# Optimization experiments

Measured on AMD Instinct MI355X. Metric: run time of the kernel, lower is better.

## Reference

```python
import jax, jax.numpy as jnp
import numpy as np

B, H, I, E = 16, 16, 512, 512  # batch, heads, input_dim, embedding_dim (I must == E for matmul(q,k))


def setup_inputs() -> dict:
    key = jax.random.key(0)
    k_x, k_q, k_k, k_v, k_w, k_b = jax.random.split(key, 6)
    return {
        "x": jax.random.normal(k_x, (B, 1, I, E), dtype=jnp.float32),
        "W_q": jax.random.normal(k_q, (1, H, I, E), dtype=jnp.float32),
        "W_k": jax.random.normal(k_k, (1, H, I, E), dtype=jnp.float32),
        "W_v": jax.random.normal(k_v, (1, H, I, E), dtype=jnp.float32),
        "mlp_w": jax.random.normal(k_w, (E, E), dtype=jnp.float32) * (1.0 / np.sqrt(E)),
        "mlp_b": jnp.zeros((E,), dtype=jnp.float32),
    }


def reference(x, W_q, W_k, W_v, mlp_w, mlp_b):
    # Broadcast elementwise "projections": [B,1,I,E] * [1,H,I,E] -> [B,H,I,E]
    q = x * W_q
    k = x * W_k
    v = x * W_v
    scale = jnp.sqrt(jnp.asarray(E, dtype=x.dtype))
    # matmul with NO transpose of keys (as in the original): [B,H,I,E]@[B,H,I,E] needs E==I
    scores = jnp.matmul(q, k) / scale            # [B,H,I,I]
    attn = jax.nn.softmax(scores, axis=2)        # softmax over dim=2 (rows), faithful to source
    emb = jnp.sum(jnp.matmul(attn, v), axis=2)   # [B,H,I,E] summed over I -> [B,H,E]
    return emb @ mlp_w.T + mlp_b                 # nn.Linear: x @ W^T + b -> [B,H,E]
```

## Files before the change

kernel.cpp:

```cpp
#include <hip/hip_runtime.h>

#define B_ 16
#define H_ 16
#define I_ 512
#define E_ 512


#define NSLICE 16
#define KSPLIT 8

__global__ __launch_bounds__(256) void k_emb_part(const float* __restrict__ x,
                                                  const float* __restrict__ Wv,
                                                  float* __restrict__ part) {
    const int etile = blockIdx.x;
    const int slice = blockIdx.y;
    const int t     = (int)threadIdx.x;
    const int lane  = t & 63;
    const int wave  = t >> 6;
    const int e     = etile * 64 + lane;
    const int b0    = (wave & 1) * 8;
    const int h0    = (wave >> 1) * 8;

    __shared__ float xs[8][16][64];
    __shared__ float ws[8][16][64];

    float acc[8][8];
#pragma unroll
    for (int bi = 0; bi < 8; ++bi)
#pragma unroll
        for (int hj = 0; hj < 8; ++hj) acc[bi][hj] = 0.0f;

    const int ibase0 = slice * 32;

    for (int chunk = 0; chunk < 4; ++chunk) {
        const int ib = ibase0 + chunk * 8;
        if (chunk) __syncthreads();
#pragma unroll
        for (int it2 = 0; it2 < 8; ++it2) {
            const int f  = t + it2 * 256;
            const int ii = f >> 8;
            const int bb = (f >> 4) & 15;
            const int eq = f & 15;
            const size_t goff = ((size_t)bb * I_ + (ib + ii)) * E_ + etile * 64 + eq * 4;
            float4 vx = *(const float4*)(x + goff);
            float4 vw = *(const float4*)(Wv + goff);
            *(float4*)&xs[ii][bb][eq * 4] = vx;
            *(float4*)&ws[ii][bb][eq * 4] = vw;
        }
        __syncthreads();

#pragma unroll
        for (int ii = 0; ii < 8; ++ii) {
            float xv[8], wv[8];
#pragma unroll
            for (int bi = 0; bi < 8; ++bi) xv[bi] = xs[ii][b0 + bi][lane];
#pragma unroll
            for (int hj = 0; hj < 8; ++hj) wv[hj] = ws[ii][h0 + hj][lane];
#pragma unroll
            for (int bi = 0; bi < 8; ++bi)
#pragma unroll
                for (int hj = 0; hj < 8; ++hj)
                    acc[bi][hj] = fmaf(xv[bi], wv[hj], acc[bi][hj]);
        }
    }

#pragma unroll
    for (int bi = 0; bi < 8; ++bi)
#pragma unroll
        for (int hj = 0; hj < 8; ++hj) {
            const int row = (b0 + bi) * H_ + h0 + hj;
            part[((size_t)slice * (B_ * H_) + row) * E_ + e] = acc[bi][hj];
        }
}

__global__ __launch_bounds__(256) void k_emb_reduce(const float4* __restrict__ part,
                                                    float4* __restrict__ emb) {
    const int idx = blockIdx.x * 256 + threadIdx.x;
    const int sl  = (B_ * H_ * E_) / 4;
    float4 s = part[idx];
#pragma unroll
    for (int j = 1; j < NSLICE; ++j) {
        float4 p = part[(size_t)j * sl + idx];
        s.x += p.x; s.y += p.y; s.z += p.z; s.w += p.w;
    }
    emb[idx] = s;
}

__global__ __launch_bounds__(256) void k_mlp_part(const float* __restrict__ emb,
                                                  const float* __restrict__ W,
                                                  float* __restrict__ part) {
    const int cblk = blockIdx.x;
    const int rblk = blockIdx.y;
    const int kch  = blockIdx.z;
    const int k0   = kch * 64;

    __shared__ float As[64][68];
    __shared__ float Ws[64][68];

    const int t = threadIdx.x;

#pragma unroll
    for (int it = 0; it < 4; ++it) {
        const int f = t + it * 256;
        const int r = f >> 4, kq = f & 15;
        float4 v = *(const float4*)(emb + (size_t)(rblk * 64 + r) * E_ + k0 + kq * 4);
        *(float4*)&As[r][((kq ^ (r >> 2)) & 15) * 4] = v;
    }
#pragma unroll
    for (int it = 0; it < 4; ++it) {
        const int f = t + it * 256;
        const int c = f >> 4, kq = f & 15;
        float4 v = *(const float4*)(W + (size_t)(cblk * 64 + c) * E_ + k0 + kq * 4);
        const int pc = (((c >> 2) ^ kq) & 15) * 4 + (c & 3);
        Ws[kq * 4 + 0][pc] = v.x;
        Ws[kq * 4 + 1][pc] = v.y;
        Ws[kq * 4 + 2][pc] = v.z;
        Ws[kq * 4 + 3][pc] = v.w;
    }
    __syncthreads();

    const int tx = t & 15, ty = t >> 4;
    const int c0 = tx * 4, r0 = ty * 4;

    float4 acc0 = {0, 0, 0, 0}, acc1 = {0, 0, 0, 0};
    float4 acc2 = {0, 0, 0, 0}, acc3 = {0, 0, 0, 0};

    for (int k = 0; k < 64; k += 4) {
        const int K  = k >> 2;
        const int ac = ((K ^ ty) & 15) * 4;
        const int wc = ((tx ^ K) & 15) * 4;
        float4 a0 = *(const float4*)&As[r0 + 0][ac];
        float4 a1 = *(const float4*)&As[r0 + 1][ac];
        float4 a2 = *(const float4*)&As[r0 + 2][ac];
        float4 a3 = *(const float4*)&As[r0 + 3][ac];
        float4 w0 = *(const float4*)&Ws[k + 0][wc];
        float4 w1 = *(const float4*)&Ws[k + 1][wc];
        float4 w2 = *(const float4*)&Ws[k + 2][wc];
        float4 w3 = *(const float4*)&Ws[k + 3][wc];
#define MLP_STEP(ACC, AV)                                                  \
        ACC.x = fmaf(AV.x, w0.x, fmaf(AV.y, w1.x, fmaf(AV.z, w2.x, fmaf(AV.w, w3.x, ACC.x)))); \
        ACC.y = fmaf(AV.x, w0.y, fmaf(AV.y, w1.y, fmaf(AV.z, w2.y, fmaf(AV.w, w3.y, ACC.y)))); \
        ACC.z = fmaf(AV.x, w0.z, fmaf(AV.y, w1.z, fmaf(AV.z, w2.z, fmaf(AV.w, w3.z, ACC.z)))); \
        ACC.w = fmaf(AV.x, w0.w, fmaf(AV.y, w1.w, fmaf(AV.z, w2.w, fmaf(AV.w, w3.w, ACC.w))));
        MLP_STEP(acc0, a0)
        MLP_STEP(acc1, a1)
        MLP_STEP(acc2, a2)
        MLP_STEP(acc3, a3)
#undef MLP_STEP
    }

    float* dst = part + ((size_t)kch * (B_ * H_) + rblk * 64 + r0) * E_ +
                 cblk * 64 + c0;
    *(float4*)(dst + 0 * E_) = acc0;
    *(float4*)(dst + 1 * E_) = acc1;
    *(float4*)(dst + 2 * E_) = acc2;
    *(float4*)(dst + 3 * E_) = acc3;
}

__global__ __launch_bounds__(256) void k_out(const float4* __restrict__ part,
                                             const float4* __restrict__ bias,
                                             float4* __restrict__ out) {
    const int idx = blockIdx.x * 256 + threadIdx.x;
    const int sl  = (B_ * H_ * E_) / 4;
    float4 s = part[idx];
#pragma unroll
    for (int j = 1; j < KSPLIT; ++j) {
        float4 p = part[(size_t)j * sl + idx];
        s.x += p.x; s.y += p.y; s.z += p.z; s.w += p.w;
    }
    float4 bv = bias[idx & (E_ / 4 - 1)];
    s.x += bv.x; s.y += bv.y; s.z += bv.z; s.w += bv.w;
    out[idx] = s;
}

extern "C" void kernel_launch(void* const* d_in, const int* in_sizes, int n_in,
                              void* d_out, int out_size, void* d_ws, size_t ws_size,
                              hipStream_t stream) {
    const float* x     = (const float*)d_in[0];
    const float* W_v   = (const float*)d_in[3];
    const float* mlp_w = (const float*)d_in[4];
    const float* mlp_b = (const float*)d_in[5];
    float* out = (float*)d_out;

    float* epart = (float*)d_ws;
    float* emb   = epart + (size_t)NSLICE * B_ * H_ * E_;
    float* mpart = emb + (size_t)B_ * H_ * E_;

    dim3 g1(E_ / 64, NSLICE);
    k_emb_part<<<g1, 256, 0, stream>>>(x, W_v, epart);

    k_emb_reduce<<<(B_ * H_ * E_ / 4) / 256, 256, 0, stream>>>(
        (const float4*)epart, (float4*)emb);

    dim3 g3(E_ / 64, (B_ * H_) / 64, KSPLIT);
    k_mlp_part<<<g3, 256, 0, stream>>>(emb, mlp_w, mpart);

    k_out<<<(B_ * H_ * E_ / 4) / 256, 256, 0, stream>>>(
        (const float4*)mpart, (const float4*)mlp_b, (float4*)out);
}
```

Baseline: 116.2 us.

## Split emb partial kernel over batch halves and drop split-K MLP reduction

The embedding partial-sum kernel gets a new grid dimension over two batch halves, doubling its block count so more CUs are busy. The cost is that each W_v tile is loaded twice and each thread holds fewer accumulators. The MLP stage loses its split-K scheme and separate reduction kernel. One kernel now loops over all of K with 32-row tiles and adds the bias directly, which removes a launch and the partial-buffer traffic. The price is only 64 blocks for the MLP, each doing a longer serial K loop.

```diff
diff --git a/kernel.cpp b/kernel.cpp
--- a/kernel.cpp
+++ b/kernel.cpp
@@ -7,59 +7,67 @@
 
 
 #define NSLICE 16
-#define KSPLIT 8
 
 __global__ __launch_bounds__(256) void k_emb_part(const float* __restrict__ x,
                                                   const float* __restrict__ Wv,
                                                   float* __restrict__ part) {
     const int etile = blockIdx.x;
-    const int slice = blockIdx.y;
+    const int b0    = blockIdx.y * 8;
+    const int slice = blockIdx.z;
     const int t     = (int)threadIdx.x;
     const int lane  = t & 63;
     const int wave  = t >> 6;
     const int e     = etile * 64 + lane;
-    const int b0    = (wave & 1) * 8;
-    const int h0    = (wave >> 1) * 8;
+    const int hw0   = wave * 4;
 
-    __shared__ float xs[8][16][64];
+    __shared__ float xs[8][8][64];
     __shared__ float ws[8][16][64];
 
-    float acc[8][8];
+    float acc[8][4];
 #pragma unroll
     for (int bi = 0; bi < 8; ++bi)
 #pragma unroll
-        for (int hj = 0; hj < 8; ++hj) acc[bi][hj] = 0.0f;
+        for (int hj = 0; hj < 4; ++hj) acc[bi][hj] = 0.0f;
 
     const int ibase0 = slice * 32;
 
     for (int chunk = 0; chunk < 4; ++chunk) {
         const int ib = ibase0 + chunk * 8;
         if (chunk) __syncthreads();
+
+#pragma unroll
+        for (int it2 = 0; it2 < 4; ++it2) {
+            const int f  = t + it2 * 256;
+            const int ii = f >> 7;
+            const int bb = (f >> 4) & 7;
+            const int eq = f & 15;
+            float4 v = *(const float4*)(
+                x + ((size_t)(b0 + bb) * I_ + (ib + ii)) * E_ + etile * 64 + eq * 4);
+            *(float4*)&xs[ii][bb][eq * 4] = v;
+        }
 #pragma unroll
         for (int it2 = 0; it2 < 8; ++it2) {
             const int f  = t + it2 * 256;
             const int ii = f >> 8;
-            const int bb = (f >> 4) & 15;
+            const int hh = (f >> 4) & 15;
             const int eq = f & 15;
-            const size_t goff = ((size_t)bb * I_ + (ib + ii)) * E_ + etile * 64 + eq * 4;
-            float4 vx = *(const float4*)(x + goff);
-            float4 vw = *(const float4*)(Wv + goff);
-            *(float4*)&xs[ii][bb][eq * 4] = vx;
-            *(float4*)&ws[ii][bb][eq * 4] = vw;
+            float4 v = *(const float4*)(
+                Wv + ((size_t)hh * I_ + (ib + ii)) * E_ + etile * 64 + eq * 4);
+            *(float4*)&ws[ii][hh][eq * 4] = v;
         }
         __syncthreads();
 
 #pragma unroll
         for (int ii = 0; ii < 8; ++ii) {
-            float xv[8], wv[8];
+            float xv[8], wv[4];
 #pragma unroll
-            for (int bi = 0; bi < 8; ++bi) xv[bi] = xs[ii][b0 + bi][lane];
+            for (int bi = 0; bi < 8; ++bi) xv[bi] = xs[ii][bi][lane];
 #pragma unroll
-            for (int hj = 0; hj < 8; ++hj) wv[hj] = ws[ii][h0 + hj][lane];
+            for (int hj = 0; hj < 4; ++hj) wv[hj] = ws[ii][hw0 + hj][lane];
 #pragma unroll
             for (int bi = 0; bi < 8; ++bi)
 #pragma unroll
-                for (int hj = 0; hj < 8; ++hj)
+                for (int hj = 0; hj < 4; ++hj)
                     acc[bi][hj] = fmaf(xv[bi], wv[hj], acc[bi][hj]);
         }
     }
@@ -67,8 +75,8 @@
 #pragma unroll
     for (int bi = 0; bi < 8; ++bi)
 #pragma unroll
-        for (int hj = 0; hj < 8; ++hj) {
-            const int row = (b0 + bi) * H_ + h0 + hj;
+        for (int hj = 0; hj < 4; ++hj) {
+            const int row = (b0 + bi) * H_ + hw0 + hj;
             part[((size_t)slice * (B_ * H_) + row) * E_ + e] = acc[bi][hj];
         }
 }
@@ -86,91 +94,74 @@
     emb[idx] = s;
 }
 
-__global__ __launch_bounds__(256) void k_mlp_part(const float* __restrict__ emb,
+__global__ __launch_bounds__(256) void k_mlp_full(const float* __restrict__ emb,
                                                   const float* __restrict__ W,
-                                                  float* __restrict__ part) {
+                                                  const float* __restrict__ bias,
+                                                  float* __restrict__ out) {
     const int cblk = blockIdx.x;
     const int rblk = blockIdx.y;
-    const int kch  = blockIdx.z;
-    const int k0   = kch * 64;
 
-    __shared__ float As[64][68];
+    __shared__ float As[32][68];
     __shared__ float Ws[64][68];
 
-    const int t = threadIdx.x;
+    const int t  = threadIdx.x;
+    const int tx = t & 15, ty = t >> 4;
+    const int c0 = tx * 4, r0 = ty * 2;
+
+    float4 acc0 = {0, 0, 0, 0}, acc1 = {0, 0, 0, 0};
+
+    for (int kc = 0; kc < 8; ++kc) {
+        const int k0 = kc * 64;
+        if (kc) __syncthreads();
 
 #pragma unroll
-    for (int it = 0; it < 4; ++it) {
-        const int f = t + it * 256;
-        const int r = f >> 4, kq = f & 15;
-        float4 v = *(const float4*)(emb + (size_t)(rblk * 64 + r) * E_ + k0 + kq * 4);
-        *(float4*)&As[r][((kq ^ (r >> 2)) & 15) * 4] = v;
-    }
+        for (int it = 0; it < 2; ++it) {
+            const int f = t + it * 256;
+            const int r = f >> 4, kq = f & 15;
+            float4 v = *(const float4*)(emb + (size_t)(rblk * 32 + r) * E_ + k0 + kq * 4);
+            *(float4*)&As[r][((kq ^ (r >> 2)) & 15) * 4] = v;
+        }
 #pragma unroll
-    for (int it = 0; it < 4; ++it) {
-        const int f = t + it * 256;
-        const int c = f >> 4, kq = f & 15;
-        float4 v = *(const float4*)(W + (size_t)(cblk * 64 + c) * E_ + k0 + kq * 4);
-        const int pc = (((c >> 2) ^ kq) & 15) * 4 + (c & 3);
-        Ws[kq * 4 + 0][pc] = v.x;
-        Ws[kq * 4 + 1][pc] = v.y;
-        Ws[kq * 4 + 2][pc] = v.z;
-        Ws[kq * 4 + 3][pc] = v.w;
-    }
-    __syncthreads();
+        for (int it = 0; it < 4; ++it) {
+            const int f = t + it * 256;
+            const int c = f >> 4, kq = f & 15;
+            float4 v = *(const float4*)(W + (size_t)(cblk * 64 + c) * E_ + k0 + kq * 4);
+            const int pc = (((c >> 2) ^ kq) & 15) * 4 + (c & 3);
+            Ws[kq * 4 + 0][pc] = v.x;
+            Ws[kq * 4 + 1][pc] = v.y;
+            Ws[kq * 4 + 2][pc] = v.z;
+            Ws[kq * 4 + 3][pc] = v.w;
+        }
+        __syncthreads();
 
-    const int tx = t & 15, ty = t >> 4;
-    const int c0 = tx * 4, r0 = ty * 4;
-
-    float4 acc0 = {0, 0, 0, 0}, acc1 = {0, 0, 0, 0};
-    float4 acc2 = {0, 0, 0, 0}, acc3 = {0, 0, 0, 0};
-
-    for (int k = 0; k < 64; k += 4) {
-        const int K  = k >> 2;
-        const int ac = ((K ^ ty) & 15) * 4;
-        const int wc = ((tx ^ K) & 15) * 4;
-        float4 a0 = *(const float4*)&As[r0 + 0][ac];
-        float4 a1 = *(const float4*)&As[r0 + 1][ac];
-        float4 a2 = *(const float4*)&As[r0 + 2][ac];
-        float4 a3 = *(const float4*)&As[r0 + 3][ac];
-        float4 w0 = *(const float4*)&Ws[k + 0][wc];
-        float4 w1 = *(const float4*)&Ws[k + 1][wc];
-        float4 w2 = *(const float4*)&Ws[k + 2][wc];
-        float4 w3 = *(const float4*)&Ws[k + 3][wc];
+        for (int k = 0; k < 64; k += 4) {
+            const int K  = k >> 2;
+            const int ac = ((K ^ (ty >> 1)) & 15) * 4;
+            const int wc = ((tx ^ K) & 15) * 4;
+            float4 a0 = *(const float4*)&As[r0 + 0][ac];
+            float4 a1 = *(const float4*)&As[r0 + 1][ac];
+            float4 w0 = *(const float4*)&Ws[k + 0][wc];
+            float4 w1 = *(const float4*)&Ws[k + 1][wc];
+            float4 w2 = *(const float4*)&Ws[k + 2][wc];
+            float4 w3 = *(const float4*)&Ws[k + 3][wc];
 #define MLP_STEP(ACC, AV)                                                  \
-        ACC.x = fmaf(AV.x, w0.x, fmaf(AV.y, w1.x, fmaf(AV.z, w2.x, fmaf(AV.w, w3.x, ACC.x)))); \
-        ACC.y = fmaf(AV.x, w0.y, fmaf(AV.y, w1.y, fmaf(AV.z, w2.y, fmaf(AV.w, w3.y, ACC.y)))); \
-        ACC.z = fmaf(AV.x, w0.z, fmaf(AV.y, w1.z, fmaf(AV.z, w2.z, fmaf(AV.w, w3.z, ACC.z)))); \
-        ACC.w = fmaf(AV.x, w0.w, fmaf(AV.y, w1.w, fmaf(AV.z, w2.w, fmaf(AV.w, w3.w, ACC.w))));
-        MLP_STEP(acc0, a0)
-        MLP_STEP(acc1, a1)
-        MLP_STEP(acc2, a2)
-        MLP_STEP(acc3, a3)
+            ACC.x = fmaf(AV.x, w0.x, fmaf(AV.y, w1.x, fmaf(AV.z, w2.x, fmaf(AV.w, w3.x, ACC.x)))); \
+            ACC.y = fmaf(AV.x, w0.y, fmaf(AV.y, w1.y, fmaf(AV.z, w2.y, fmaf(AV.w, w3.y, ACC.y)))); \
+            ACC.z = fmaf(AV.x, w0.z, fmaf(AV.y, w1.z, fmaf(AV.z, w2.z, fmaf(AV.w, w3.z, ACC.z)))); \
+            ACC.w = fmaf(AV.x, w0.w, fmaf(AV.y, w1.w, fmaf(AV.z, w2.w, fmaf(AV.w, w3.w, ACC.w))));
+            MLP_STEP(acc0, a0)
+            MLP_STEP(acc1, a1)
 #undef MLP_STEP
+        }
     }
 
-    float* dst = part + ((size_t)kch * (B_ * H_) + rblk * 64 + r0) * E_ +
-                 cblk * 64 + c0;
-    *(float4*)(dst + 0 * E_) = acc0;
-    *(float4*)(dst + 1 * E_) = acc1;
-    *(float4*)(dst + 2 * E_) = acc2;
-    *(float4*)(dst + 3 * E_) = acc3;
-}
+    const float4 bv = *(const float4*)(bias + cblk * 64 + c0);
+    acc0.x += bv.x; acc0.y += bv.y; acc0.z += bv.z; acc0.w += bv.w;
+    acc1.x += bv.x; acc1.y += bv.y; acc1.z += bv.z; acc1.w += bv.w;
 
-__global__ __launch_bounds__(256) void k_out(const float4* __restrict__ part,
-                                             const float4* __restrict__ bias,
-                                             float4* __restrict__ out) {
-    const int idx = blockIdx.x * 256 + threadIdx.x;
-    const int sl  = (B_ * H_ * E_) / 4;
-    float4 s = part[idx];
-#pragma unroll
-    for (int j = 1; j < KSPLIT; ++j) {
-        float4 p = part[(size_t)j * sl + idx];
-        s.x += p.x; s.y += p.y; s.z += p.z; s.w += p.w;
-    }
-    float4 bv = bias[idx & (E_ / 4 - 1)];
-    s.x += bv.x; s.y += bv.y; s.z += bv.z; s.w += bv.w;
-    out[idx] = s;
+    float* o = out + (size_t)(rblk * 32 + r0) * E_ + cblk * 64 + c0;
+    *(float4*)(o + 0 * E_) = acc0;
+    *(float4*)(o + 1 * E_) = acc1;
 }
 
 extern "C" void kernel_launch(void* const* d_in, const int* in_sizes, int n_in,
@@ -184,17 +175,13 @@
 
     float* epart = (float*)d_ws;
     float* emb   = epart + (size_t)NSLICE * B_ * H_ * E_;
-    float* mpart = emb + (size_t)B_ * H_ * E_;
 
-    dim3 g1(E_ / 64, NSLICE);
+    dim3 g1(E_ / 64, 2, NSLICE);
     k_emb_part<<<g1, 256, 0, stream>>>(x, W_v, epart);
 
     k_emb_reduce<<<(B_ * H_ * E_ / 4) / 256, 256, 0, stream>>>(
         (const float4*)epart, (float4*)emb);
 
-    dim3 g3(E_ / 64, (B_ * H_) / 64, KSPLIT);
-    k_mlp_part<<<g3, 256, 0, stream>>>(emb, mlp_w, mpart);
-
-    k_out<<<(B_ * H_ * E_ / 4) / 256, 256, 0, stream>>>(
-        (const float4*)mpart, (const float4*)mlp_b, (float4*)out);
+    dim3 g3(E_ / 64, (B_ * H_) / 32);
+    k_mlp_full<<<g3, 256, 0, stream>>>(emb, mlp_w, mlp_b, out);
 }
```

Result: slower. 131.7 us (+13.3%).
